# Kernel tuning notes

Measured on AMD Instinct MI355X. Metric: run time of the kernel, lower is better.

Reference implementation:

```python
import jax, jax.numpy as jnp
import numpy as np

N_NODES = 10000
N_EDGES = 320000
D_FEAT = 256
N_LAYERS = 4
EPS = 1e-16


def setup_inputs() -> dict:
    key = jax.random.key(0)
    k1, k2, k3 = jax.random.split(key, 3)
    feats = jax.random.normal(k1, (N_NODES, D_FEAT), dtype=jnp.float32)
    src = jax.random.randint(k2, (N_EDGES,), 0, N_NODES, dtype=jnp.int32)
    dst = jax.random.randint(k3, (N_EDGES,), 0, N_NODES, dtype=jnp.int32)
    betas = jnp.ones((N_LAYERS,), dtype=jnp.float32)  # agnn_conv_init_beta = 1.0
    return {"feats": feats, "src": src, "dst": dst, "betas": betas}


def _agnn_layer(h, src, dst, beta, num_nodes):
    # cosine-similarity edge attention (DGL AGNNConv): normalize node feats, dot per edge
    h_norm = h * jax.lax.rsqrt(jnp.sum(h * h, axis=-1, keepdims=True) + EPS)  # [N, d]
    cos = jnp.sum(h_norm[src] * h_norm[dst], axis=-1)                          # [E]
    logits = beta * cos                                                        # [E]
    # edge softmax over incoming edges of each destination node
    m = jax.ops.segment_max(logits, dst, num_segments=num_nodes)               # [N]
    ex = jnp.exp(logits - m[dst])                                              # [E]
    denom = jax.ops.segment_sum(ex, dst, num_segments=num_nodes)               # [N]
    alpha = ex / (denom[dst] + EPS)                                            # [E]
    # scatter-aggregate weighted neighbor features
    msg = alpha[:, None] * h[src]                                              # [E, d]
    return jax.ops.segment_sum(msg, dst, num_segments=num_nodes)               # [N, d]


def reference(feats, src, dst, betas):
    h = feats
    num_nodes = feats.shape[0]
    for i in range(N_LAYERS):
        h = _agnn_layer(h, src, dst, betas[i], num_nodes)
        h = jax.nn.relu(h)
    return h
```

## Files before the change

### kernel.cpp

```cpp
#include <hip/hip_runtime.h>
#include <hip/hip_bf16.h>

#define NN 10000
#define NE 320000
#define D 256
#define D4 64
#define BH 128
#define EPB (NE / BH)


template<int CTRL>
__device__ __forceinline__ float dpp_add(float x) {
    int y = __builtin_amdgcn_update_dpp(0, __float_as_int(x), CTRL, 0xF, 0xF, true);
    return x + __int_as_float(y);
}

__device__ __forceinline__ float wave_red_sum(float x) {
    x = dpp_add<0x111>(x);
    x = dpp_add<0x112>(x);
    x = dpp_add<0x114>(x);
    x = dpp_add<0x118>(x);
    x = dpp_add<0x142>(x);
    x = dpp_add<0x143>(x);
    return __int_as_float(__builtin_amdgcn_readlane(__float_as_int(x), 63));
}

__device__ __forceinline__ float bcast_lane_f(float x, int t) {
    return __int_as_float(__builtin_amdgcn_readlane(__float_as_int(x), t));
}


__global__ void hist_rank_kernel(const int* __restrict__ dst,
                                 int* __restrict__ blockhist, int* __restrict__ rank) {
    __shared__ int lh[NN];
    for (int i = threadIdx.x; i < NN; i += 256) lh[i] = 0;
    __syncthreads();
    int e0 = blockIdx.x * EPB, e1 = e0 + EPB;
    for (int e = e0 + threadIdx.x; e < e1; e += 256)
        rank[e] = atomicAdd(&lh[dst[e]], 1);
    __syncthreads();
    int* bh = blockhist + blockIdx.x * NN;
    for (int i = threadIdx.x; i < NN; i += 256) bh[i] = lh[i];
}

__global__ void colscan_kernel(int* __restrict__ blockhist, int* __restrict__ cnt, int n) {
    int d = blockIdx.x * blockDim.x + threadIdx.x;
    if (d >= n) return;
    int run = 0;
    for (int b = 0; b < BH; ++b) {
        int v = blockhist[b * NN + d];
        blockhist[b * NN + d] = run;
        run += v;
    }
    cnt[d] = run;
}

__global__ void scan_kernel(const int* __restrict__ cnt, int* __restrict__ rowptr, int n) {
    __shared__ int part[256];
    int t = threadIdx.x;
    int chunk = (n + 255) / 256;
    int b = t * chunk;
    int e = b + chunk; if (e > n) e = n;
    int s = 0;
    for (int i = b; i < e; ++i) s += cnt[i];
    part[t] = s;
    __syncthreads();
    for (int off = 1; off < 256; off <<= 1) {
        int v = (t >= off) ? part[t - off] : 0;
        __syncthreads();
        part[t] += v;
        __syncthreads();
    }
    int acc = part[t] - s;
    for (int i = b; i < e; ++i) { rowptr[i] = acc; acc += cnt[i]; }
    if (e == n && b < n) rowptr[n] = acc;
}

__global__ void scatter2_kernel(const int* __restrict__ src, const int* __restrict__ dst,
                                const int* __restrict__ rank, const int* __restrict__ blockhist,
                                const int* __restrict__ rowptr, int* __restrict__ esrc, int nE) {
    int e = blockIdx.x * blockDim.x + threadIdx.x;
    if (e >= nE) return;
    int b = e / EPB;
    int d = dst[e];
    esrc[rowptr[d] + blockhist[b * NN + d] + rank[e]] = src[e];
}


__global__ void norm_kernel(const float4* __restrict__ h, float* __restrict__ inv, int n) {
    int wid  = (blockIdx.x * blockDim.x + threadIdx.x) >> 6;
    int lane = threadIdx.x & 63;
    if (wid >= n) return;
    float4 v = h[wid * D4 + lane];
    float s = wave_red_sum(v.x * v.x + v.y * v.y + v.z * v.z + v.w * v.w);
    if (lane == 0) inv[wid] = rsqrtf(s + 1e-16f);
}


__device__ __forceinline__ float dot4(float4 a, float4 b) {
    return a.x * b.x + a.y * b.y + a.z * b.z + a.w * b.w;
}

__global__ void fused_kernel(const float4* __restrict__ h, const float* __restrict__ inv,
                             float* __restrict__ invN,
                             const int* __restrict__ rowptr, const int* __restrict__ esrc,
                             const float* __restrict__ betas, int layer,
                             float4* __restrict__ out, int n) {
    int wid  = (blockIdx.x * blockDim.x + threadIdx.x) >> 6;
    int lane = threadIdx.x & 63;
    if (wid >= n) return;

    float4 a    = h[wid * D4 + lane];
    float  bivd = betas[layer] * inv[wid];
    int beg = rowptr[wid], end = rowptr[wid + 1];

    float4 acc = make_float4(0.f, 0.f, 0.f, 0.f);
    float dsum = 0.f;

    for (int base = beg; base < end; base += 64) {
        int idx = base + lane;
        int s_l = 0; float iv_l = 0.f;
        if (idx < end) { s_l = esrc[idx]; iv_l = inv[s_l]; }
        int m = end - base; if (m > 64) m = 64;

        int t = 0;
        for (; t + 3 < m; t += 4) {
            int s0 = __builtin_amdgcn_readlane(s_l, t);
            int s1 = __builtin_amdgcn_readlane(s_l, t + 1);
            int s2 = __builtin_amdgcn_readlane(s_l, t + 2);
            int s3 = __builtin_amdgcn_readlane(s_l, t + 3);
            float4 v0 = h[s0 * D4 + lane];
            float4 v1 = h[s1 * D4 + lane];
            float4 v2 = h[s2 * D4 + lane];
            float4 v3 = h[s3 * D4 + lane];
            float i0 = bcast_lane_f(iv_l, t);
            float i1 = bcast_lane_f(iv_l, t + 1);
            float i2 = bcast_lane_f(iv_l, t + 2);
            float i3 = bcast_lane_f(iv_l, t + 3);
            float p0 = wave_red_sum(dot4(a, v0));
            float p1 = wave_red_sum(dot4(a, v1));
            float p2 = wave_red_sum(dot4(a, v2));
            float p3 = wave_red_sum(dot4(a, v3));
            float e0 = __expf(p0 * bivd * i0);
            float e1 = __expf(p1 * bivd * i1);
            float e2 = __expf(p2 * bivd * i2);
            float e3 = __expf(p3 * bivd * i3);
            dsum += (e0 + e1) + (e2 + e3);
            acc.x += e0 * v0.x + e1 * v1.x + e2 * v2.x + e3 * v3.x;
            acc.y += e0 * v0.y + e1 * v1.y + e2 * v2.y + e3 * v3.y;
            acc.z += e0 * v0.z + e1 * v1.z + e2 * v2.z + e3 * v3.z;
            acc.w += e0 * v0.w + e1 * v1.w + e2 * v2.w + e3 * v3.w;
        }
        for (; t < m; ++t) {
            int   s0 = __builtin_amdgcn_readlane(s_l, t);
            float i0 = bcast_lane_f(iv_l, t);
            float4 v0 = h[s0 * D4 + lane];
            float p0 = wave_red_sum(dot4(a, v0));
            float e0 = __expf(p0 * bivd * i0);
            dsum += e0;
            acc.x += e0 * v0.x; acc.y += e0 * v0.y;
            acc.z += e0 * v0.z; acc.w += e0 * v0.w;
        }
    }

    float r = 1.f / (dsum + 1e-16f);
    float4 w2;
    w2.x = fmaxf(acc.x * r, 0.f); w2.y = fmaxf(acc.y * r, 0.f);
    w2.z = fmaxf(acc.z * r, 0.f); w2.w = fmaxf(acc.w * r, 0.f);
    out[wid * D4 + lane] = w2;

    float s = wave_red_sum(dot4(w2, w2));
    if (lane == 0) invN[wid] = rsqrtf(s + 1e-16f);
}


extern "C" void kernel_launch(void* const* d_in, const int* in_sizes, int n_in,
                              void* d_out, int out_size, void* d_ws, size_t ws_size,
                              hipStream_t stream) {
    const float* feats = (const float*)d_in[0];
    const int*   src   = (const int*)d_in[1];
    const int*   dst   = (const int*)d_in[2];
    const float* betas = (const float*)d_in[3];
    float* out = (float*)d_out;

    float* hA        = (float*)d_ws;
    float* hB        = hA + NN * D;
    float* inv0      = hB + NN * D;
    float* inv1      = inv0 + NN;
    int*   rowptr    = (int*)(inv1 + NN);
    int*   cnt       = rowptr + (NN + 1);
    int*   esrc      = cnt + NN;
    int*   rank      = esrc + NE;
    int*   blockhist = rank + NE;

    hist_rank_kernel<<<BH, 256, 0, stream>>>(dst, blockhist, rank);
    colscan_kernel<<<(NN + 255) / 256, 256, 0, stream>>>(blockhist, cnt, NN);
    scan_kernel<<<1, 256, 0, stream>>>(cnt, rowptr, NN);
    scatter2_kernel<<<(NE + 255) / 256, 256, 0, stream>>>(src, dst, rank, blockhist,
                                                          rowptr, esrc, NE);

    norm_kernel<<<(NN * 64 + 255) / 256, 256, 0, stream>>>((const float4*)feats, inv0, NN);

    const int node_blocks = (NN * 64 + 255) / 256;

    const float* hin = feats;
    float* invCur = inv0;
    float* invNxt = inv1;
    for (int l = 0; l < 4; ++l) {
        float* hout = (l == 3) ? out : ((l & 1) ? hB : hA);
        fused_kernel<<<node_blocks, 256, 0, stream>>>((const float4*)hin, invCur, invNxt,
                                                      rowptr, esrc, betas, l,
                                                      (float4*)hout, NN);
        hin = hout;
        float* tmp = invCur; invCur = invNxt; invNxt = tmp;
    }
}
```

Before: 191.9 us.

## Store normalized node features in fp16 and process two edges per wave

Each node's features are now kept pre-normalized in fp16 together with a separate fp32 norm, which halves the bytes of every neighbor gather. Each wave splits into two 32-lane halves that handle different edges concurrently, and the next group's gathers are prefetched while the current group is computed. The norm is folded back into the aggregation weight, and the two halves are combined with a cross-half shuffle at the end. This risks accuracy loss from fp16 storage of the features across four layers.

```diff
diff --git a/kernel.cpp b/kernel.cpp
--- a/kernel.cpp
+++ b/kernel.cpp
@@ -1,10 +1,9 @@
 #include <hip/hip_runtime.h>
-#include <hip/hip_bf16.h>
+#include <hip/hip_fp16.h>
 
 #define NN 10000
 #define NE 320000
 #define D 256
-#define D4 64
 #define BH 128
 #define EPB (NE / BH)
 
@@ -15,18 +14,28 @@
     return x + __int_as_float(y);
 }
 
-__device__ __forceinline__ float wave_red_sum(float x) {
+__device__ __forceinline__ float red32(float x) {
     x = dpp_add<0x111>(x);
     x = dpp_add<0x112>(x);
     x = dpp_add<0x114>(x);
     x = dpp_add<0x118>(x);
     x = dpp_add<0x142>(x);
-    x = dpp_add<0x143>(x);
-    return __int_as_float(__builtin_amdgcn_readlane(__float_as_int(x), 63));
-}
-
-__device__ __forceinline__ float bcast_lane_f(float x, int t) {
+    return x;
+}
+
+__device__ __forceinline__ float rl_f(float x, int t) {
     return __int_as_float(__builtin_amdgcn_readlane(__float_as_int(x), t));
+}
+
+union H2U { __half2 h; unsigned u; };
+
+__device__ __forceinline__ void unpack8(uint4 r, float* v) {
+    H2U a, b, c, d; a.u = r.x; b.u = r.y; c.u = r.z; d.u = r.w;
+    float2 f;
+    f = __half22float2(a.h); v[0] = f.x; v[1] = f.y;
+    f = __half22float2(b.h); v[2] = f.x; v[3] = f.y;
+    f = __half22float2(c.h); v[4] = f.x; v[5] = f.y;
+    f = __half22float2(d.h); v[6] = f.x; v[7] = f.y;
 }
 
 
@@ -87,90 +96,133 @@
 }
 
 
-__global__ void norm_kernel(const float4* __restrict__ h, float* __restrict__ inv, int n) {
+__global__ void norm_kernel(const float4* __restrict__ h, uint2* __restrict__ hn,
+                            float* __restrict__ nrm, int n) {
     int wid  = (blockIdx.x * blockDim.x + threadIdx.x) >> 6;
     int lane = threadIdx.x & 63;
     if (wid >= n) return;
-    float4 v = h[wid * D4 + lane];
-    float s = wave_red_sum(v.x * v.x + v.y * v.y + v.z * v.z + v.w * v.w);
-    if (lane == 0) inv[wid] = rsqrtf(s + 1e-16f);
-}
-
-
-__device__ __forceinline__ float dot4(float4 a, float4 b) {
-    return a.x * b.x + a.y * b.y + a.z * b.z + a.w * b.w;
-}
-
-__global__ void fused_kernel(const float4* __restrict__ h, const float* __restrict__ inv,
-                             float* __restrict__ invN,
-                             const int* __restrict__ rowptr, const int* __restrict__ esrc,
-                             const float* __restrict__ betas, int layer,
-                             float4* __restrict__ out, int n) {
+    float4 v = h[wid * 64 + lane];
+    float s = red32(v.x * v.x + v.y * v.y + v.z * v.z + v.w * v.w);
+    float tot = rl_f(s, 31) + rl_f(s, 63);
+    float rs = rsqrtf(tot + 1e-16f);
+    H2U u0, u1;
+    u0.h = __floats2half2_rn(v.x * rs, v.y * rs);
+    u1.h = __floats2half2_rn(v.z * rs, v.w * rs);
+    hn[wid * 64 + lane] = make_uint2(u0.u, u1.u);
+    if (lane == 0) nrm[wid] = 1.0f / rs;
+}
+
+
+__global__ __launch_bounds__(256, 6)
+void fused_kernel(const uint4* __restrict__ hnin, const float* __restrict__ nrmin,
+                  const int* __restrict__ rowptr, const int* __restrict__ esrc,
+                  const float* __restrict__ betas, int layer,
+                  float4* __restrict__ outf, uint4* __restrict__ hnout,
+                  float* __restrict__ nrmout, int lastLayer, int n) {
     int wid  = (blockIdx.x * blockDim.x + threadIdx.x) >> 6;
     int lane = threadIdx.x & 63;
     if (wid >= n) return;
-
-    float4 a    = h[wid * D4 + lane];
-    float  bivd = betas[layer] * inv[wid];
+    int q = lane & 31;
+    bool hiHalf = lane >= 32;
+
+    float a[8];
+    unpack8(hnin[wid * 32 + q], a);
+    float beta = betas[layer];
+
     int beg = rowptr[wid], end = rowptr[wid + 1];
-
-    float4 acc = make_float4(0.f, 0.f, 0.f, 0.f);
+    float acc[8] = {0, 0, 0, 0, 0, 0, 0, 0};
     float dsum = 0.f;
 
     for (int base = beg; base < end; base += 64) {
         int idx = base + lane;
-        int s_l = 0; float iv_l = 0.f;
-        if (idx < end) { s_l = esrc[idx]; iv_l = inv[s_l]; }
+        int s_l = 0; float nm_l = 0.f;
+        if (idx < end) { s_l = esrc[idx]; nm_l = nrmin[s_l]; }
         int m = end - base; if (m > 64) m = 64;
 
-        int t = 0;
-        for (; t + 3 < m; t += 4) {
-            int s0 = __builtin_amdgcn_readlane(s_l, t);
-            int s1 = __builtin_amdgcn_readlane(s_l, t + 1);
-            int s2 = __builtin_amdgcn_readlane(s_l, t + 2);
-            int s3 = __builtin_amdgcn_readlane(s_l, t + 3);
-            float4 v0 = h[s0 * D4 + lane];
-            float4 v1 = h[s1 * D4 + lane];
-            float4 v2 = h[s2 * D4 + lane];
-            float4 v3 = h[s3 * D4 + lane];
-            float i0 = bcast_lane_f(iv_l, t);
-            float i1 = bcast_lane_f(iv_l, t + 1);
-            float i2 = bcast_lane_f(iv_l, t + 2);
-            float i3 = bcast_lane_f(iv_l, t + 3);
-            float p0 = wave_red_sum(dot4(a, v0));
-            float p1 = wave_red_sum(dot4(a, v1));
-            float p2 = wave_red_sum(dot4(a, v2));
-            float p3 = wave_red_sum(dot4(a, v3));
-            float e0 = __expf(p0 * bivd * i0);
-            float e1 = __expf(p1 * bivd * i1);
-            float e2 = __expf(p2 * bivd * i2);
-            float e3 = __expf(p3 * bivd * i3);
-            dsum += (e0 + e1) + (e2 + e3);
-            acc.x += e0 * v0.x + e1 * v1.x + e2 * v2.x + e3 * v3.x;
-            acc.y += e0 * v0.y + e1 * v1.y + e2 * v2.y + e3 * v3.y;
-            acc.z += e0 * v0.z + e1 * v1.z + e2 * v2.z + e3 * v3.z;
-            acc.w += e0 * v0.w + e1 * v1.w + e2 * v2.w + e3 * v3.w;
-        }
-        for (; t < m; ++t) {
-            int   s0 = __builtin_amdgcn_readlane(s_l, t);
-            float i0 = bcast_lane_f(iv_l, t);
-            float4 v0 = h[s0 * D4 + lane];
-            float p0 = wave_red_sum(dot4(a, v0));
-            float e0 = __expf(p0 * bivd * i0);
-            dsum += e0;
-            acc.x += e0 * v0.x; acc.y += e0 * v0.y;
-            acc.z += e0 * v0.z; acc.w += e0 * v0.w;
-        }
-    }
+        int nf = m & ~3;
+        uint4 b0, b1;
+        if (nf > 0) {
+            int sA = __builtin_amdgcn_readlane(s_l, 0);
+            int sB = __builtin_amdgcn_readlane(s_l, 1);
+            int sC = __builtin_amdgcn_readlane(s_l, 2);
+            int sD = __builtin_amdgcn_readlane(s_l, 3);
+            b0 = hnin[(hiHalf ? sB : sA) * 32 + q];
+            b1 = hnin[(hiHalf ? sD : sC) * 32 + q];
+        }
+        for (int g = 0; g < nf; g += 4) {
+            float v0[8], v1[8];
+            unpack8(b0, v0);
+            unpack8(b1, v1);
+            float nmA = rl_f(nm_l, g),     nmB = rl_f(nm_l, g + 1);
+            float nmC = rl_f(nm_l, g + 2), nmD = rl_f(nm_l, g + 3);
+            int gn = g + 4;
+            if (gn < nf) {
+                int sA = __builtin_amdgcn_readlane(s_l, gn);
+                int sB = __builtin_amdgcn_readlane(s_l, gn + 1);
+                int sC = __builtin_amdgcn_readlane(s_l, gn + 2);
+                int sD = __builtin_amdgcn_readlane(s_l, gn + 3);
+                b0 = hnin[(hiHalf ? sB : sA) * 32 + q];
+                b1 = hnin[(hiHalf ? sD : sC) * 32 + q];
+            }
+            float p0 = 0.f, p1 = 0.f;
+            #pragma unroll
+            for (int j = 0; j < 8; ++j) { p0 += a[j] * v0[j]; p1 += a[j] * v1[j]; }
+            p0 = red32(p0); p1 = red32(p1);
+            float xA = __expf(beta * rl_f(p0, 31));
+            float xB = __expf(beta * rl_f(p0, 63));
+            float xC = __expf(beta * rl_f(p1, 31));
+            float xD = __expf(beta * rl_f(p1, 63));
+            dsum += (xA + xB) + (xC + xD);
+            float e0 = hiHalf ? xB * nmB : xA * nmA;
+            float e1 = hiHalf ? xD * nmD : xC * nmC;
+            #pragma unroll
+            for (int j = 0; j < 8; ++j) acc[j] += e0 * v0[j] + e1 * v1[j];
+        }
+        for (int t = nf; t < m; ++t) {
+            int   sA  = __builtin_amdgcn_readlane(s_l, t);
+            float nmA = rl_f(nm_l, t);
+            float v0[8]; unpack8(hnin[sA * 32 + q], v0);
+            float p0 = 0.f;
+            #pragma unroll
+            for (int j = 0; j < 8; ++j) p0 += a[j] * v0[j];
+            p0 = red32(p0);
+            float xA = __expf(beta * rl_f(p0, 31));
+            dsum += xA;
+            float e0 = hiHalf ? 0.f : xA * nmA;
+            #pragma unroll
+            for (int j = 0; j < 8; ++j) acc[j] += e0 * v0[j];
+        }
+    }
+
+    #pragma unroll
+    for (int j = 0; j < 8; ++j) acc[j] += __shfl_xor(acc[j], 32);
 
     float r = 1.f / (dsum + 1e-16f);
-    float4 w2;
-    w2.x = fmaxf(acc.x * r, 0.f); w2.y = fmaxf(acc.y * r, 0.f);
-    w2.z = fmaxf(acc.z * r, 0.f); w2.w = fmaxf(acc.w * r, 0.f);
-    out[wid * D4 + lane] = w2;
-
-    float s = wave_red_sum(dot4(w2, w2));
-    if (lane == 0) invN[wid] = rsqrtf(s + 1e-16f);
+    float w[8];
+    float ss = 0.f;
+    #pragma unroll
+    for (int j = 0; j < 8; ++j) {
+        w[j] = fmaxf(acc[j] * r, 0.f);
+        ss += w[j] * w[j];
+    }
+    ss = red32(ss);
+    float ssum = rl_f(ss, 31);
+    float rs = rsqrtf(ssum + 1e-16f);
+
+    if (!hiHalf) {
+        if (lastLayer) {
+            outf[wid * 64 + q * 2]     = make_float4(w[0], w[1], w[2], w[3]);
+            outf[wid * 64 + q * 2 + 1] = make_float4(w[4], w[5], w[6], w[7]);
+        } else {
+            H2U u0, u1, u2, u3;
+            u0.h = __floats2half2_rn(w[0] * rs, w[1] * rs);
+            u1.h = __floats2half2_rn(w[2] * rs, w[3] * rs);
+            u2.h = __floats2half2_rn(w[4] * rs, w[5] * rs);
+            u3.h = __floats2half2_rn(w[6] * rs, w[7] * rs);
+            hnout[wid * 32 + q] = make_uint4(u0.u, u1.u, u2.u, u3.u);
+            if (lane == 0) nrmout[wid] = 1.0f / rs;
+        }
+    }
 }
 
 
@@ -183,11 +235,11 @@
     const float* betas = (const float*)d_in[3];
     float* out = (float*)d_out;
 
-    float* hA        = (float*)d_ws;
-    float* hB        = hA + NN * D;
-    float* inv0      = hB + NN * D;
-    float* inv1      = inv0 + NN;
-    int*   rowptr    = (int*)(inv1 + NN);
+    uint4* hn0       = (uint4*)d_ws;
+    uint4* hn1       = hn0 + NN * 32;
+    float* nrm0      = (float*)(hn1 + NN * 32);
+    float* nrm1      = nrm0 + NN;
+    int*   rowptr    = (int*)(nrm1 + NN);
     int*   cnt       = rowptr + (NN + 1);
     int*   esrc      = cnt + NN;
     int*   rank      = esrc + NE;
@@ -199,19 +251,21 @@
     scatter2_kernel<<<(NE + 255) / 256, 256, 0, stream>>>(src, dst, rank, blockhist,
                                                           rowptr, esrc, NE);
 
-    norm_kernel<<<(NN * 64 + 255) / 256, 256, 0, stream>>>((const float4*)feats, inv0, NN);
-
-    const int node_blocks = (NN * 64 + 255) / 256;
-
-    const float* hin = feats;
-    float* invCur = inv0;
-    float* invNxt = inv1;
+    norm_kernel<<<(NN * 64 + 255) / 256, 256, 0, stream>>>((const float4*)feats,
+                                                           (uint2*)hn0, nrm0, NN);
+
+    const int node_blocks = (NN + 3) / 4;
+
+    const uint4* hnin = hn0;
+    const float* nrmin = nrm0;
     for (int l = 0; l < 4; ++l) {
-        float* hout = (l == 3) ? out : ((l & 1) ? hB : hA);
-        fused_kernel<<<node_blocks, 256, 0, stream>>>((const float4*)hin, invCur, invNxt,
-                                                      rowptr, esrc, betas, l,
-                                                      (float4*)hout, NN);
-        hin = hout;
-        float* tmp = invCur; invCur = invNxt; invNxt = tmp;
-    }
-}
+        uint4* hnout  = (l & 1) ? hn0 : hn1;
+        float* nrmout = (l & 1) ? nrm0 : nrm1;
+        fused_kernel<<<node_blocks, 256, 0, stream>>>(hnin, nrmin, rowptr, esrc,
+                                                      betas, l, (float4*)out,
+                                                      hnout, nrmout,
+                                                      (l == 3) ? 1 : 0, NN);
+        hnin = hnout;
+        nrmin = nrmout;
+    }
+}
```

After: 157.5 us. 1.22x faster.
